# Kernel tuning notes

Hardware: AMD Instinct MI355X
Metric: run time of the kernel (lower is better)

## Reference

```python
import jax, jax.numpy as jnp
import numpy as np

DIM = 3072
HEADS = 24
HEAD_DIM = 128
INNER = HEADS * HEAD_DIM
EPS = 1e-6
B, IMG_LEN, TXT_LEN = 1, 2048, 512
S = IMG_LEN + TXT_LEN


def setup_inputs() -> dict:
    key = jax.random.key(0)
    ks = jax.random.split(key, 16)
    w = lambda k, shp: (jax.random.normal(k, shp, dtype=jnp.float32) * 0.02)
    return {
        "x": jax.random.normal(ks[0], (B, IMG_LEN, DIM), dtype=jnp.float32),
        "ctx": jax.random.normal(ks[1], (B, TXT_LEN, DIM), dtype=jnp.float32),
        "rope_cos": jax.random.uniform(ks[2], (S, HEAD_DIM), dtype=jnp.float32),
        "rope_sin": jax.random.uniform(ks[3], (S, HEAD_DIM), dtype=jnp.float32),
        "wq": w(ks[4], (INNER, DIM)),
        "wk": w(ks[5], (INNER, DIM)),
        "wv": w(ks[6], (INNER, DIM)),
        "gq": jnp.ones((HEAD_DIM,), jnp.float32),
        "gk": jnp.ones((HEAD_DIM,), jnp.float32),
        "wo": w(ks[7], (DIM, INNER)),
        "awq": w(ks[8], (INNER, DIM)),
        "awk": w(ks[9], (INNER, DIM)),
        "awv": w(ks[10], (INNER, DIM)),
        "agq": jnp.ones((HEAD_DIM,), jnp.float32),
        "agk": jnp.ones((HEAD_DIM,), jnp.float32),
        "awo": w(ks[11], (DIM, INNER)),
    }


def _rms_norm(t, g):
    # t: [b, s, h, d]; normalize over last dim
    var = jnp.mean(t * t, axis=-1, keepdims=True)
    return t * jax.lax.rsqrt(var + EPS) * g


def _heads(t):
    # [b, s, h*d] -> [b, s, h, d]
    b, s, _ = t.shape
    return t.reshape(b, s, HEADS, HEAD_DIM)


def _apply_rope(t, cos, sin):
    # t: [b, s, h, d]; cos/sin: [s, d] interleaved-pair layout (diffusers Flux style)
    b, s, h, d = t.shape
    x = t.reshape(b, s, h, d // 2, 2)
    rot = jnp.stack([-x[..., 1], x[..., 0]], axis=-1).reshape(b, s, h, d)
    c = cos[None, :, None, :]
    si = sin[None, :, None, :]
    return t * c + rot * si


def reference(x, ctx, rope_cos, rope_sin, wq, wk, wv, gq, gk, wo,
              awq, awk, awv, agq, agk, awo):
    # image-stream QKV + per-head RMSNorm on q,k
    q = _rms_norm(_heads(x @ wq.T), gq)
    k = _rms_norm(_heads(x @ wk.T), gk)
    v = _heads(x @ wv.T)
    # context-stream QKV
    qc = _rms_norm(_heads(ctx @ awq.T), agq)
    kc = _rms_norm(_heads(ctx @ awk.T), agk)
    vc = _heads(ctx @ awv.T)
    # joint streams: [ctx, img] ordering (out[:, :txt_len] is context)
    q = jnp.concatenate([qc, q], axis=1)
    k = jnp.concatenate([kc, k], axis=1)
    v = jnp.concatenate([vc, v], axis=1)
    q = _apply_rope(q, rope_cos, rope_sin)
    k = _apply_rope(k, rope_cos, rope_sin)
    # SDPA
    scale = 1.0 / jnp.sqrt(jnp.float32(HEAD_DIM))
    scores = jnp.einsum('bqhd,bkhd->bhqk', q, k) * scale
    probs = jax.nn.softmax(scores, axis=-1)
    out = jnp.einsum('bhqk,bkhd->bqhd', probs, v)
    out = out.reshape(out.shape[0], out.shape[1], INNER)
    img_out = out[:, TXT_LEN:] @ wo.T
    txt_out = out[:, :TXT_LEN] @ awo.T
    return (img_out, txt_out)
```

## Files before the change

### kernel.cpp

```cpp
#include <hip/hip_runtime.h>
#include <hip/hip_bf16.h>

#define DIMC 3072
#define NHEADS 24
#define HD 128
#define SEQ 2560
#define TXTLEN 512
#define IMGLEN 2048

using short8 = __attribute__((ext_vector_type(8))) short;
using f32x4  = __attribute__((ext_vector_type(4))) float;

static __device__ __forceinline__ float bf2f(unsigned short u) {
    unsigned v = ((unsigned)u) << 16;
    return __builtin_bit_cast(float, v);
}
static __device__ __forceinline__ unsigned short f2bf(float f) {
    unsigned u = __builtin_bit_cast(unsigned, f);
    return (unsigned short)((u + 0x7FFFu + ((u >> 16) & 1u)) >> 16);
}
static __device__ __forceinline__ void gload16(const void* g, void* l) {
    __builtin_amdgcn_global_load_lds((const __attribute__((address_space(1))) unsigned int*)g,
                                     (__attribute__((address_space(3))) unsigned int*)l,
                                     16, 0, 0);
}

__global__ __launch_bounds__(256)
void castk(const float* __restrict__ in, unsigned short* __restrict__ out, int n8)
{
    const int i = blockIdx.x * 256 + threadIdx.x;
    if (i >= n8) return;
    const float4 a = *reinterpret_cast<const float4*>(in + (size_t)i * 8);
    const float4 b = *reinterpret_cast<const float4*>(in + (size_t)i * 8 + 4);
    short8 o;
    o[0] = (short)f2bf(a.x); o[1] = (short)f2bf(a.y);
    o[2] = (short)f2bf(a.z); o[3] = (short)f2bf(a.w);
    o[4] = (short)f2bf(b.x); o[5] = (short)f2bf(b.y);
    o[6] = (short)f2bf(b.z); o[7] = (short)f2bf(b.w);
    *reinterpret_cast<short8*>(out + (size_t)i * 8) = o;
}

struct W8 { const float* src[8]; };
__global__ __launch_bounds__(256)
void castw(W8 a, unsigned short* __restrict__ dstbase, int n8, size_t wsz)
{
    const int i = blockIdx.x * 256 + threadIdx.x;
    if (i >= n8) return;
    const float* in = a.src[blockIdx.y];
    unsigned short* out = dstbase + (size_t)blockIdx.y * wsz;
    const float4 av = *reinterpret_cast<const float4*>(in + (size_t)i * 8);
    const float4 bv = *reinterpret_cast<const float4*>(in + (size_t)i * 8 + 4);
    short8 o;
    o[0] = (short)f2bf(av.x); o[1] = (short)f2bf(av.y);
    o[2] = (short)f2bf(av.z); o[3] = (short)f2bf(av.w);
    o[4] = (short)f2bf(bv.x); o[5] = (short)f2bf(bv.y);
    o[6] = (short)f2bf(bv.z); o[7] = (short)f2bf(bv.w);
    *reinterpret_cast<short8*>(out + (size_t)i * 8) = o;
}

struct QkvArgs {
    const unsigned short* A;
    const unsigned short* w0[3];
    const unsigned short* w1[3];
    unsigned short* c[3];
};

__global__ __launch_bounds__(512)
void gemm_qkv(QkvArgs args)
{
    __shared__ unsigned short As[2][256 * 64];
    __shared__ unsigned short Bs[2][192 * 64];

    const int bid = blockIdx.x;
    const int swz = (bid & 7) * 60 + (bid >> 3);
    const int which = swz / 160;
    const int rem = swz - which * 160;
    const int bn = rem / 10;
    const int bm = rem - bn * 10;

    const int rowbase = bm * 256, colbase = bn * 192;
    const unsigned short* __restrict__ A = args.A;
    const unsigned short* __restrict__ W = (rowbase < TXTLEN) ? args.w0[which] : args.w1[which];
    unsigned short* __restrict__ C = args.c[which];

    const int t = threadIdx.x, l = t & 63;
    const int w = t >> 6;
    const int lr = l & 15, lk = l >> 4;
    const int wm = w >> 2, wn = w & 3;

    f32x4 acc[8][3] = {};

    const int srow = t >> 3;
    const int gsl  = ((t & 7) ^ (srow & 7)) * 8;
    const int dst0 = srow * 64 + (t & 7) * 8;

    const unsigned short* AgR[4];
    const unsigned short* WgR[3];
#pragma unroll
    for (int r = 0; r < 4; ++r)
        AgR[r] = A + (size_t)(rowbase + r * 64 + srow) * DIMC + gsl;
#pragma unroll
    for (int r = 0; r < 3; ++r)
        WgR[r] = W + (size_t)(colbase + r * 64 + srow) * DIMC + gsl;

    auto SA2 = [&](unsigned short* dst, int r, int k0) {
        gload16(AgR[r] + k0, dst + r * 4096 + dst0);
    };
    auto SB2 = [&](unsigned short* dst, int r, int k0) {
        gload16(WgR[r] + k0, dst + r * 4096 + dst0);
    };

    const int xsl0 = ((lk)     ^ (lr & 7)) * 8;
    const int xsl1 = ((lk + 4) ^ (lr & 7)) * 8;
    const int arow = wm * 128 + lr;
    const int brow = wn * 48 + lr;

    constexpr int NT = DIMC / 64;
    constexpr int ITERS = NT / 2;

#pragma unroll
    for (int r = 0; r < 4; ++r) SA2(&As[0][0], r, 0);
#pragma unroll
    for (int r = 0; r < 3; ++r) SB2(&Bs[0][0], r, 0);
#pragma unroll
    for (int r = 0; r < 3; ++r) SB2(&Bs[1][0], r, 64);

    auto HALF = [&](int CB, int kA, int kB) {
        unsigned short* Ab  = &As[CB][0];
        unsigned short* Bb  = &Bs[CB][0];
        unsigned short* Aot = &As[CB ^ 1][0];
        short8 bfr[3][2];
#pragma unroll
        for (int q = 0; q < 4; ++q) {
            if (q == 0) {
                asm volatile("s_waitcnt vmcnt(3)" ::: "memory");
            }
            __builtin_amdgcn_s_barrier();
            if (q == 0) {
#pragma unroll
                for (int nf = 0; nf < 3; ++nf) {
                    bfr[nf][0] = *reinterpret_cast<const short8*>(&Bb[(brow + nf * 16) * 64 + xsl0]);
                    bfr[nf][1] = *reinterpret_cast<const short8*>(&Bb[(brow + nf * 16) * 64 + xsl1]);
                }
            }
            short8 afr[2][2];
#pragma unroll
            for (int i = 0; i < 2; ++i) {
                afr[i][0] = *reinterpret_cast<const short8*>(&Ab[(arow + (2 * q + i) * 16) * 64 + xsl0]);
                afr[i][1] = *reinterpret_cast<const short8*>(&Ab[(arow + (2 * q + i) * 16) * 64 + xsl1]);
            }
            if (q == 0)      { SA2(Aot, 0, kA); SA2(Aot, 1, kA); }
            else if (q == 1) { SA2(Aot, 2, kA); SA2(Aot, 3, kA); }
            else if (q == 2) { SB2(Bb,  0, kB); SB2(Bb,  1, kB); }
            else             { SB2(Bb,  2, kB); }

            __builtin_amdgcn_s_setprio(1);
#pragma unroll
            for (int i = 0; i < 2; ++i)
#pragma unroll
                for (int nf = 0; nf < 3; ++nf) {
                    acc[2 * q + i][nf] = __builtin_amdgcn_mfma_f32_16x16x32_bf16(
                        afr[i][0], bfr[nf][0], acc[2 * q + i][nf], 0, 0, 0);
                    acc[2 * q + i][nf] = __builtin_amdgcn_mfma_f32_16x16x32_bf16(
                        afr[i][1], bfr[nf][1], acc[2 * q + i][nf], 0, 0, 0);
                }
            __builtin_amdgcn_s_setprio(0);
        }
    };

    for (int it = 0; it < ITERS; ++it) {
        const int t2 = 2 * it + 2 < NT ? 2 * it + 2 : NT - 1;
        const int t3 = 2 * it + 3 < NT ? 2 * it + 3 : NT - 1;
        HALF(0, (2 * it + 1) * 64, t2 * 64);
        HALF(1, t2 * 64,           t3 * 64);
    }

    asm volatile("s_waitcnt vmcnt(0)" ::: "memory");
    __builtin_amdgcn_s_barrier();

#pragma unroll
    for (int mf = 0; mf < 8; ++mf) {
#pragma unroll
        for (int r = 0; r < 4; ++r) {
            const int row = rowbase + wm * 128 + mf * 16 + lk * 4 + r;
            unsigned short* crow = C + (size_t)row * DIMC + colbase + wn * 48;
#pragma unroll
            for (int nf = 0; nf < 3; ++nf)
                crow[nf * 16 + lr] = f2bf(acc[mf][nf][r]);
        }
    }
}

__global__ __launch_bounds__(256)
void gemm_out(const unsigned short* __restrict__ A, const unsigned short* __restrict__ W0,
              const unsigned short* __restrict__ W1, float* __restrict__ Ctxt,
              float* __restrict__ Cimg)
{
    __shared__ unsigned short As[3][128 * 32];
    __shared__ unsigned short Bs[3][128 * 32];

    const int bid = blockIdx.x;
    const int swz = (bid & 7) * 60 + (bid >> 3);
    const int bm = swz % 20;
    const int bn = swz / 20;

    const int rowbase = bm * 128, colbase = bn * 128;
    const unsigned short* __restrict__ W = (rowbase < TXTLEN) ? W0 : W1;

    const int t = threadIdx.x, w = t >> 6, l = t & 63;
    const int lr = l & 15, lk = l >> 4;
    const int wr = (w >> 1) * 64, wc = (w & 1) * 64;

    f32x4 acc[4][4] = {};

    const int ssl = ((l & 3) ^ ((l >> 3) & 3)) * 8;
    const unsigned short* Ag = A + (size_t)(rowbase + w * 32 + (l >> 2)) * DIMC + ssl;
    const unsigned short* Wg = W + (size_t)(colbase + w * 32 + (l >> 2)) * DIMC + ssl;

    auto STAGE = [&](int buf, int k0) {
        gload16(Ag + k0,             &As[buf][w * 1024]);
        gload16(Ag + 16 * DIMC + k0, &As[buf][w * 1024 + 512]);
        gload16(Wg + k0,             &Bs[buf][w * 1024]);
        gload16(Wg + 16 * DIMC + k0, &Bs[buf][w * 1024 + 512]);
    };

    constexpr int NIT = DIMC / 32;
    STAGE(0, 0);
    STAGE(1, 32);

    const int rsl = (lk ^ ((lr >> 1) & 3)) * 8;
    int buf = 0;
    for (int it = 0; it < NIT; ++it) {
        asm volatile("s_waitcnt vmcnt(4)" ::: "memory");
        __builtin_amdgcn_s_barrier();
        asm volatile("" ::: "memory");

        {
            const int k2 = (it + 2 < NIT) ? (it + 2) : (NIT - 1);
            int b2 = buf + 2; if (b2 >= 3) b2 -= 3;
            STAGE(b2, k2 * 32);
        }

        short8 af[4], bf[4];
#pragma unroll
        for (int m = 0; m < 4; ++m)
            af[m] = *reinterpret_cast<const short8*>(&As[buf][(wr + m * 16 + lr) * 32 + rsl]);
#pragma unroll
        for (int n = 0; n < 4; ++n)
            bf[n] = *reinterpret_cast<const short8*>(&Bs[buf][(wc + n * 16 + lr) * 32 + rsl]);

        __builtin_amdgcn_s_setprio(1);
#pragma unroll
        for (int m = 0; m < 4; ++m)
#pragma unroll
            for (int n = 0; n < 4; ++n)
                acc[m][n] = __builtin_amdgcn_mfma_f32_16x16x32_bf16(af[m], bf[n], acc[m][n], 0, 0, 0);
        __builtin_amdgcn_s_setprio(0);

        buf = (buf + 1 == 3) ? 0 : buf + 1;
    }

    float* Cb; int rloc;
    if (rowbase < TXTLEN) { Cb = Ctxt; rloc = rowbase; }
    else                  { Cb = Cimg; rloc = rowbase - TXTLEN; }
#pragma unroll
    for (int m = 0; m < 4; ++m) {
#pragma unroll
        for (int r = 0; r < 4; ++r) {
            const int row = rloc + wr + m * 16 + lk * 4 + r;
            float* crow = Cb + (size_t)row * DIMC + colbase + wc;
#pragma unroll
            for (int n = 0; n < 4; ++n)
                crow[n * 16 + lr] = acc[m][n][r];
        }
    }
}

__global__ __launch_bounds__(256)
void normrope(unsigned short* __restrict__ Q, unsigned short* __restrict__ K,
              const float* __restrict__ gq, const float* __restrict__ gk,
              const float* __restrict__ agq, const float* __restrict__ agk,
              const float* __restrict__ rc, const float* __restrict__ rs)
{
    const int wid  = (blockIdx.x << 2) + (threadIdx.x >> 6);
    const int lane = threadIdx.x & 63;
    const int s = wid / NHEADS, h = wid - s * NHEADS;
    const bool img = (s >= TXTLEN);
    const float* gq_ = img ? gq : agq;
    const float* gk_ = img ? gk : agk;

    const size_t base = (size_t)s * DIMC + h * HD + lane * 2;
    const float2 c2  = *reinterpret_cast<const float2*>(rc + (size_t)s * HD + lane * 2);
    const float2 s2  = *reinterpret_cast<const float2*>(rs + (size_t)s * HD + lane * 2);
    const float2 gqv = *reinterpret_cast<const float2*>(gq_ + lane * 2);
    const float2 gkv = *reinterpret_cast<const float2*>(gk_ + lane * 2);

    {
        unsigned pr = *reinterpret_cast<unsigned*>(Q + base);
        float vx = bf2f((unsigned short)(pr & 0xffff));
        float vy = bf2f((unsigned short)(pr >> 16));
        float ss = vx * vx + vy * vy;
#pragma unroll
        for (int off = 1; off < 64; off <<= 1) ss += __shfl_xor(ss, off);
        const float rr = rsqrtf(ss * (1.f / HD) + 1e-6f);
        const float txv = vx * rr * gqv.x, tyv = vy * rr * gqv.y;
        const float qs = 0.08838834764831845f;
        const float ox = (txv * c2.x - tyv * s2.x) * qs;
        const float oy = (tyv * c2.y + txv * s2.y) * qs;
        *reinterpret_cast<unsigned*>(Q + base) = (unsigned)f2bf(ox) | ((unsigned)f2bf(oy) << 16);
    }
    {
        unsigned pr = *reinterpret_cast<unsigned*>(K + base);
        float vx = bf2f((unsigned short)(pr & 0xffff));
        float vy = bf2f((unsigned short)(pr >> 16));
        float ss = vx * vx + vy * vy;
#pragma unroll
        for (int off = 1; off < 64; off <<= 1) ss += __shfl_xor(ss, off);
        const float rr = rsqrtf(ss * (1.f / HD) + 1e-6f);
        const float txv = vx * rr * gkv.x, tyv = vy * rr * gkv.y;
        const float ox = txv * c2.x - tyv * s2.x;
        const float oy = tyv * c2.y + txv * s2.y;
        *reinterpret_cast<unsigned*>(K + base) = (unsigned)f2bf(ox) | ((unsigned)f2bf(oy) << 16);
    }
}

__global__ __launch_bounds__(256)
void transpose_v(const unsigned short* __restrict__ V, unsigned short* __restrict__ Vt)
{
    __shared__ unsigned short Ts[64][136];
    const int kt = blockIdx.x, h = blockIdx.y;
    const int t = threadIdx.x;
#pragma unroll
    for (int p = 0; p < 4; ++p) {
        const int row = p * 16 + (t >> 4);
        const int col = (t & 15) * 8;
        *reinterpret_cast<short8*>(&Ts[row][col]) =
            *reinterpret_cast<const short8*>(V + (size_t)(kt * 64 + row) * DIMC + h * HD + col);
    }
    __syncthreads();
    const int d = t >> 1, kh = t & 1;
    unsigned short* dst = Vt + (size_t)h * HD * SEQ + (size_t)d * SEQ + kt * 64 + kh * 32;
#pragma unroll
    for (int j4 = 0; j4 < 4; ++j4) {
        short8 o;
#pragma unroll
        for (int j = 0; j < 8; ++j) o[j] = (short)Ts[kh * 32 + j4 * 8 + j][d];
        *reinterpret_cast<short8*>(dst + j4 * 8) = o;
    }
}

__global__ __launch_bounds__(512)
void attn_mfma(const unsigned short* __restrict__ Q, const unsigned short* __restrict__ K,
               const unsigned short* __restrict__ Vt, unsigned short* __restrict__ O)
{
    __shared__ unsigned short Ks[2][64 * 128];
    __shared__ unsigned short Vs[2][128 * 64];
    __shared__ unsigned short Ps[8][16 * 64];

    const int bid = blockIdx.x;
    const int swz = (bid & 7) * 60 + (bid >> 3);
    const int bq = swz % 20;
    const int h  = swz / 20;

    const int t = threadIdx.x, w = t >> 6, l = t & 63;
    const int lr = l & 15, lk = l >> 4;
    const int q0 = bq * 128 + w * 16;

    short8 qf[4];
#pragma unroll
    for (int kk = 0; kk < 4; ++kk)
        qf[kk] = *reinterpret_cast<const short8*>(
            Q + (size_t)(q0 + lr) * DIMC + h * HD + kk * 32 + lk * 8);

    f32x4 oacc[8] = {};
    float mrow[4] = {-1e30f, -1e30f, -1e30f, -1e30f};
    float lrow[4] = {};

    const unsigned short* Kg[2];
    const unsigned short* Vg[2];
#pragma unroll
    for (int i = 0; i < 2; ++i) {
        const int kr = w * 8 + i * 4 + (l >> 4);
        Kg[i] = K + (size_t)kr * DIMC + h * HD + (((l & 15) ^ (kr & 7)) * 8);
        const int vr = w * 16 + i * 8 + (l >> 3);
        Vg[i] = Vt + (size_t)h * HD * SEQ + (size_t)vr * SEQ + (((l & 7) ^ (vr & 7)) * 8);
    }

    auto STAGE = [&](int buf, int kv0) {
#pragma unroll
        for (int i = 0; i < 2; ++i) {
            gload16(Kg[i] + (size_t)kv0 * DIMC, &Ks[buf][(w * 8 + i * 4) * 128]);
            gload16(Vg[i] + kv0,                &Vs[buf][(w * 16 + i * 8) * 64]);
        }
    };

    STAGE(0, 0);

    constexpr int NT = SEQ / 64;
    for (int kt = 0; kt < NT; ++kt) {
        const int buf = kt & 1;
        __syncthreads();
        if (kt + 1 < NT) STAGE(buf ^ 1, (kt + 1) * 64);

        f32x4 sf[4] = {};
        __builtin_amdgcn_s_setprio(1);
#pragma unroll
        for (int nf = 0; nf < 4; ++nf) {
            const int row = nf * 16 + lr;
            const int sw = (row & 7) << 3;
#pragma unroll
            for (int kk = 0; kk < 4; ++kk) {
                short8 bfr = *reinterpret_cast<const short8*>(
                    &Ks[buf][row * 128 + ((kk * 32 + lk * 8) ^ sw)]);
                sf[nf] = __builtin_amdgcn_mfma_f32_16x16x32_bf16(qf[kk], bfr, sf[nf], 0, 0, 0);
            }
        }
        __builtin_amdgcn_s_setprio(0);

        float mxr[4];
#pragma unroll
        for (int r = 0; r < 4; ++r) {
            float mx = fmaxf(fmaxf(sf[0][r], sf[1][r]), fmaxf(sf[2][r], sf[3][r]));
#pragma unroll
            for (int off = 1; off < 16; off <<= 1) mx = fmaxf(mx, __shfl_xor(mx, off));
            mxr[r] = mx;
        }
        const float need = fmaxf(fmaxf(mxr[0] - mrow[0], mxr[1] - mrow[1]),
                                 fmaxf(mxr[2] - mrow[2], mxr[3] - mrow[3]));
        if (!__all(need <= 8.0f)) {
#pragma unroll
            for (int r = 0; r < 4; ++r) {
                const float mn = fmaxf(mrow[r], mxr[r]);
                const float alpha = __expf(mrow[r] - mn);
                mrow[r] = mn;
                lrow[r] *= alpha;
#pragma unroll
                for (int nf = 0; nf < 8; ++nf) oacc[nf][r] *= alpha;
            }
        }
#pragma unroll
        for (int r = 0; r < 4; ++r) {
            float ps = 0.f;
#pragma unroll
            for (int nf = 0; nf < 4; ++nf) {
                const float p = __expf(sf[nf][r] - mrow[r]);
                sf[nf][r] = p;
                ps += p;
            }
#pragma unroll
            for (int off = 1; off < 16; off <<= 1) ps += __shfl_xor(ps, off);
            lrow[r] += ps;
        }

#pragma unroll
        for (int r = 0; r < 4; ++r) {
            const int prow = lk * 4 + r;
            const int sw = (prow & 7) << 3;
#pragma unroll
            for (int nf = 0; nf < 4; ++nf) {
                const int col = nf * 16 + lr;
                Ps[w][prow * 64 + (col ^ sw)] = f2bf(sf[nf][r]);
            }
        }

        __builtin_amdgcn_s_setprio(1);
#pragma unroll
        for (int ks = 0; ks < 2; ++ks) {
            short8 pa = *reinterpret_cast<const short8*>(
                &Ps[w][lr * 64 + ((ks * 32 + lk * 8) ^ ((lr & 7) << 3))]);
#pragma unroll
            for (int nf = 0; nf < 8; ++nf) {
                const int vrow = nf * 16 + lr;
                short8 vf = *reinterpret_cast<const short8*>(
                    &Vs[buf][vrow * 64 + ((ks * 32 + lk * 8) ^ ((vrow & 7) << 3))]);
                oacc[nf] = __builtin_amdgcn_mfma_f32_16x16x32_bf16(pa, vf, oacc[nf], 0, 0, 0);
            }
        }
        __builtin_amdgcn_s_setprio(0);
    }

    float inv[4];
#pragma unroll
    for (int r = 0; r < 4; ++r) inv[r] = 1.f / lrow[r];
#pragma unroll
    for (int nf = 0; nf < 8; ++nf)
#pragma unroll
        for (int r = 0; r < 4; ++r)
            O[(size_t)(q0 + lk * 4 + r) * DIMC + h * HD + nf * 16 + lr] = f2bf(oacc[nf][r] * inv[r]);
}

extern "C" void kernel_launch(void* const* d_in, const int* in_sizes, int n_in,
                              void* d_out, int out_size, void* d_ws, size_t ws_size,
                              hipStream_t stream)
{
    const float* x    = (const float*)d_in[0];
    const float* ctx  = (const float*)d_in[1];
    const float* rc   = (const float*)d_in[2];
    const float* rs   = (const float*)d_in[3];
    const float* wq   = (const float*)d_in[4];
    const float* wk   = (const float*)d_in[5];
    const float* wv   = (const float*)d_in[6];
    const float* gq   = (const float*)d_in[7];
    const float* gk   = (const float*)d_in[8];
    const float* wo   = (const float*)d_in[9];
    const float* awq  = (const float*)d_in[10];
    const float* awk  = (const float*)d_in[11];
    const float* awv  = (const float*)d_in[12];
    const float* agq  = (const float*)d_in[13];
    const float* agk  = (const float*)d_in[14];
    const float* awo  = (const float*)d_in[15];

    unsigned short* wsp = (unsigned short*)d_ws;
    const size_t SZ  = (size_t)SEQ * DIMC;
    const size_t WSZ = (size_t)DIMC * DIMC;
    unsigned short* XC  = wsp;
    unsigned short* Qb  = XC + SZ;
    unsigned short* Kb  = Qb + SZ;
    unsigned short* Vb  = Kb + SZ;
    unsigned short* Vtb = Vb + SZ;
    unsigned short* Ob  = Vtb + SZ;
    unsigned short* Wc  = Ob + SZ;

    {
        int n8 = (int)((size_t)TXTLEN * DIMC / 8);
        castk<<<dim3((n8 + 255) / 256), dim3(256), 0, stream>>>(ctx, XC, n8);
        n8 = (int)((size_t)IMGLEN * DIMC / 8);
        castk<<<dim3((n8 + 255) / 256), dim3(256), 0, stream>>>(x, XC + (size_t)TXTLEN * DIMC, n8);
    }
    {
        W8 w8;
        w8.src[0] = awq; w8.src[1] = wq; w8.src[2] = awk; w8.src[3] = wk;
        w8.src[4] = awv; w8.src[5] = wv; w8.src[6] = awo; w8.src[7] = wo;
        const int n8 = (int)(WSZ / 8);
        castw<<<dim3((n8 + 255) / 256, 8), dim3(256), 0, stream>>>(w8, Wc, n8, WSZ);
    }

    QkvArgs qa;
    qa.A = XC;
    qa.w0[0] = Wc + 0 * WSZ; qa.w1[0] = Wc + 1 * WSZ; qa.c[0] = Qb;
    qa.w0[1] = Wc + 2 * WSZ; qa.w1[1] = Wc + 3 * WSZ; qa.c[1] = Kb;
    qa.w0[2] = Wc + 4 * WSZ; qa.w1[2] = Wc + 5 * WSZ; qa.c[2] = Vb;
    gemm_qkv<<<dim3(480), dim3(512), 0, stream>>>(qa);

    normrope<<<dim3(SEQ * NHEADS / 4), dim3(256), 0, stream>>>(Qb, Kb, gq, gk, agq, agk, rc, rs);

    transpose_v<<<dim3(SEQ / 64, NHEADS), dim3(256), 0, stream>>>(Vb, Vtb);

    attn_mfma<<<dim3(480), dim3(512), 0, stream>>>(Qb, Kb, Vtb, Ob);

    float* out = (float*)d_out;
    gemm_out<<<dim3(480), dim3(256), 0, stream>>>(
        Ob, Wc + 6 * WSZ, Wc + 7 * WSZ, out + (size_t)IMGLEN * DIMC, out);
}
```

Baseline: 537.0 us.

## Triple-buffer B tiles in QKV GEMM and use one barrier per k-tile

Reworks the gemm_qkv main loop from a two-tile unrolled HALF scheme into a single k-tile loop. A stays double-buffered while B moves to a three-slot ring that is prefetched two tiles ahead. All global-to-LDS loads for the next tiles are now issued right after one wait and barrier at the top of each tile, instead of spreading loads and four barriers across the sub-steps. This cuts barrier overhead and lengthens B prefetch distance, at the cost of more LDS (a third B buffer) and less spreading of load issue among the MFMA work.

```diff
diff --git a/kernel.cpp b/kernel.cpp
--- a/kernel.cpp
+++ b/kernel.cpp
@@ -69,7 +69,7 @@
 void gemm_qkv(QkvArgs args)
 {
     __shared__ unsigned short As[2][256 * 64];
-    __shared__ unsigned short Bs[2][192 * 64];
+    __shared__ unsigned short Bs[3][192 * 64];
 
     const int bid = blockIdx.x;
     const int swz = (bid & 7) * 60 + (bid >> 3);
@@ -116,7 +116,6 @@
     const int brow = wn * 48 + lr;
 
     constexpr int NT = DIMC / 64;
-    constexpr int ITERS = NT / 2;
 
 #pragma unroll
     for (int r = 0; r < 4; ++r) SA2(&As[0][0], r, 0);
@@ -125,35 +124,42 @@
 #pragma unroll
     for (int r = 0; r < 3; ++r) SB2(&Bs[1][0], r, 64);
 
-    auto HALF = [&](int CB, int kA, int kB) {
-        unsigned short* Ab  = &As[CB][0];
-        unsigned short* Bb  = &Bs[CB][0];
-        unsigned short* Aot = &As[CB ^ 1][0];
+    int ab = 0;
+    int bcur = 0;
+    for (int kt = 0; kt < NT; ++kt) {
+        asm volatile("s_waitcnt vmcnt(3)" ::: "memory");
+        __builtin_amdgcn_s_barrier();
+
+        {
+            const int tA = (kt + 1 < NT) ? kt + 1 : NT - 1;
+            const int tB = (kt + 2 < NT) ? kt + 2 : NT - 1;
+            int b2 = bcur + 2; if (b2 >= 3) b2 -= 3;
+            unsigned short* Anext = &As[ab ^ 1][0];
+            unsigned short* Bnext = &Bs[b2][0];
+#pragma unroll
+            for (int r = 0; r < 4; ++r) SA2(Anext, r, tA * 64);
+#pragma unroll
+            for (int r = 0; r < 3; ++r) SB2(Bnext, r, tB * 64);
+        }
+
+        unsigned short* Ab = &As[ab][0];
+        unsigned short* Bb = &Bs[bcur][0];
+
         short8 bfr[3][2];
 #pragma unroll
+        for (int nf = 0; nf < 3; ++nf) {
+            bfr[nf][0] = *reinterpret_cast<const short8*>(&Bb[(brow + nf * 16) * 64 + xsl0]);
+            bfr[nf][1] = *reinterpret_cast<const short8*>(&Bb[(brow + nf * 16) * 64 + xsl1]);
+        }
+
+#pragma unroll
         for (int q = 0; q < 4; ++q) {
-            if (q == 0) {
-                asm volatile("s_waitcnt vmcnt(3)" ::: "memory");
-            }
-            __builtin_amdgcn_s_barrier();
-            if (q == 0) {
-#pragma unroll
-                for (int nf = 0; nf < 3; ++nf) {
-                    bfr[nf][0] = *reinterpret_cast<const short8*>(&Bb[(brow + nf * 16) * 64 + xsl0]);
-                    bfr[nf][1] = *reinterpret_cast<const short8*>(&Bb[(brow + nf * 16) * 64 + xsl1]);
-                }
-            }
             short8 afr[2][2];
 #pragma unroll
             for (int i = 0; i < 2; ++i) {
                 afr[i][0] = *reinterpret_cast<const short8*>(&Ab[(arow + (2 * q + i) * 16) * 64 + xsl0]);
                 afr[i][1] = *reinterpret_cast<const short8*>(&Ab[(arow + (2 * q + i) * 16) * 64 + xsl1]);
             }
-            if (q == 0)      { SA2(Aot, 0, kA); SA2(Aot, 1, kA); }
-            else if (q == 1) { SA2(Aot, 2, kA); SA2(Aot, 3, kA); }
-            else if (q == 2) { SB2(Bb,  0, kB); SB2(Bb,  1, kB); }
-            else             { SB2(Bb,  2, kB); }
-
             __builtin_amdgcn_s_setprio(1);
 #pragma unroll
             for (int i = 0; i < 2; ++i)
@@ -166,17 +172,10 @@
                 }
             __builtin_amdgcn_s_setprio(0);
         }
-    };
-
-    for (int it = 0; it < ITERS; ++it) {
-        const int t2 = 2 * it + 2 < NT ? 2 * it + 2 : NT - 1;
-        const int t3 = 2 * it + 3 < NT ? 2 * it + 3 : NT - 1;
-        HALF(0, (2 * it + 1) * 64, t2 * 64);
-        HALF(1, t2 * 64,           t3 * 64);
-    }
-
-    asm volatile("s_waitcnt vmcnt(0)" ::: "memory");
-    __builtin_amdgcn_s_barrier();
+
+        ab ^= 1;
+        bcur = (bcur + 1 == 3) ? 0 : bcur + 1;
+    }
 
 #pragma unroll
     for (int mf = 0; mf < 8; ++mf) {
```

Result: no change. 546.8 us (+1.8%).
